# Kernel tuning notes

Hardware: AMD Instinct MI355X
Metric: run time of the kernel (lower is better)

Reference implementation:

```python
import jax, jax.numpy as jnp
import numpy as np

LANE_WEIGHT = 1.0   # _LANE_LOSS_WEIGHT
TEMP = 0.1          # args.score_temp

B, L, K, T = 256, 16, 64, 50
NL, NT = B * L, B * L * K


def _seg_ids(starts, n):
    # contiguous segments covering [0, n): segment id = (# starts <= i) - 1
    return (jnp.cumsum(jnp.zeros((n,), jnp.int32).at[starts].add(1)) - 1).astype(jnp.int32)


def _seg_log_softmax(x, seg, nseg):
    m = jax.ops.segment_max(x, seg, num_segments=nseg)
    z = x - m[seg]
    lse = jnp.log(jax.ops.segment_sum(jnp.exp(z), seg, num_segments=nseg))
    return z - lse[seg]


def _seg_softmax(x, seg, nseg):
    m = jax.ops.segment_max(x, seg, num_segments=nseg)
    e = jnp.exp(x - m[seg])
    s = jax.ops.segment_sum(e, seg, num_segments=nseg)
    return e / s[seg]


def setup_inputs() -> dict:
    key = jax.random.key(0)
    k1, k2, k3, k4, k5 = jax.random.split(key, 5)
    lane_scores = jax.random.normal(k1, (NL,), jnp.float32)
    traj_scores = jax.random.normal(k2, (NT, 1), jnp.float32)
    pred_candidates = jax.random.normal(k3, (NT, T, 2), jnp.float32)
    pred_gt = jax.random.normal(k4, (B, T, 2), jnp.float32)
    scales = jnp.ones((B,), jnp.float32)
    # ragged segment boundaries (here uniform, but reference only uses starts)
    cls_start_end_idx = jnp.stack([jnp.arange(B, dtype=jnp.int32) * L,
                                   jnp.arange(B, dtype=jnp.int32) * L + L], axis=1)
    trajs_start_end_idx = jnp.stack([jnp.arange(NL, dtype=jnp.int32) * K,
                                     jnp.arange(NL, dtype=jnp.int32) * K + K], axis=1)
    cls_oracle = jax.random.bernoulli(k5, 0.3, (NL,))
    # guarantee >= 1 oracle lane per sample (original divides by len(traj_loss))
    cls_oracle = cls_oracle.at[jnp.arange(B) * L].set(True)
    return {
        "lane_scores": lane_scores,
        "traj_scores": traj_scores,
        "pred_candidates": pred_candidates,
        "pred_gt": pred_gt,
        "scales": scales,
        "cls_oracle": cls_oracle,
        "cls_start_end_idx": cls_start_end_idx,
        "trajs_start_end_idx": trajs_start_end_idx,
    }


def reference(lane_scores, traj_scores, pred_candidates, pred_gt, scales,
              cls_oracle, cls_start_end_idx, trajs_start_end_idx):
    nl, nt = lane_scores.shape[0], traj_scores.shape[0]
    b = cls_start_end_idx.shape[0]
    lane_sample = _seg_ids(cls_start_end_idx[:, 0], nl)   # [NL] -> sample id
    traj_lane = _seg_ids(trajs_start_end_idx[:, 0], nt)   # [NT] -> lane id
    traj_sample = lane_sample[traj_lane]                  # [NT] -> sample id

    # ---- lane-level cross entropy per sample ----
    oracle_f = cls_oracle.astype(lane_scores.dtype)
    oracle_per_sample = jax.ops.segment_sum(oracle_f, lane_sample, num_segments=b)
    lane_target = oracle_f / oracle_per_sample[lane_sample]
    lane_logp = _seg_log_softmax(lane_scores, lane_sample, b)
    lane_loss = jax.ops.segment_sum(-lane_target * lane_logp, lane_sample,
                                    num_segments=b) * LANE_WEIGHT  # [B]

    # ---- trajectory-level cross entropy per oracle lane ----
    # ScoreEvaluator.scoring_trajs: ADE distance to GT, scale-normalized, negated
    diff = pred_candidates - pred_gt[traj_sample]          # [NT, T, 2]
    ade = jnp.mean(jnp.sqrt(jnp.sum(diff * diff, axis=-1) + 1e-12), axis=-1)
    scores = -ade / scales[traj_sample]                    # [NT]

    target = _seg_softmax(scores / TEMP, traj_lane, nl)    # softmax(scores/temp)
    out_logp = _seg_log_softmax(traj_scores[:, 0], traj_lane, nl)
    ce_per_lane = jax.ops.segment_sum(-target * out_logp, traj_lane,
                                      num_segments=nl)     # [NL]
    # only oracle lanes contribute; average over oracle-lane count per sample
    traj_loss = jax.ops.segment_sum(ce_per_lane * oracle_f, lane_sample,
                                    num_segments=b) / oracle_per_sample  # [B]

    return jnp.mean(lane_loss + traj_loss)
```

## Files before the change

### kernel.cpp

```cpp
#include <hip/hip_runtime.h>
#include <math.h>


#define LANE_WEIGHT 1.0f
#define TEMP_INV    10.0f

__global__ __launch_bounds__(256) void lane_ce_kernel(
    const float* __restrict__ pred_candidates,
    const float* __restrict__ pred_gt,
    const float* __restrict__ traj_scores,
    const float* __restrict__ scales,
    const int*   __restrict__ cls_se,
    const int*   __restrict__ trajs_se,
    float*       __restrict__ ws_ce,
    int B, int T)
{
    const int lane = blockIdx.x;
    const int tid  = threadIdx.x;

    __shared__ int    s_sample;
    __shared__ float4 s_gt4[64];
    __shared__ float  s_acc[64];

    if (tid == 0) {
        int lo = 0, hi = B - 1;
        while (lo < hi) {
            int mid = (lo + hi + 1) >> 1;
            if (cls_se[2 * mid] <= lane) lo = mid; else hi = mid - 1;
        }
        s_sample = lo;
    }
    __syncthreads();
    const int sample = s_sample;
    const int t0 = trajs_se[2 * lane];
    const int t1 = trajs_se[2 * lane + 1];
    const int Kl = t1 - t0;

    float* s_gt = (float*)s_gt4;
    for (int i = tid; i < T * 2; i += blockDim.x)
        s_gt[i] = pred_gt[(size_t)sample * (T * 2) + i];
    __syncthreads();

    const int tl = tid >> 2;
    const int q  = tid & 3;
    float partial = 0.0f;
    if (tl < Kl) {
        const float4* base =
            (const float4*)(pred_candidates + (size_t)(t0 + tl) * (T * 2));
        const int nf4 = T / 2;
        for (int r = q; r < nf4; r += 4) {
            float4 c = base[r];
            float4 g = s_gt4[r];
            float dx0 = c.x - g.x, dy0 = c.y - g.y;
            float dx1 = c.z - g.z, dy1 = c.w - g.w;
            partial += sqrtf(dx0 * dx0 + dy0 * dy0 + 1e-12f)
                     + sqrtf(dx1 * dx1 + dy1 * dy1 + 1e-12f);
        }
    }
    partial += __shfl_xor(partial, 1);
    partial += __shfl_xor(partial, 2);
    if (q == 0 && tl < Kl) s_acc[tl] = partial;
    __syncthreads();

    if (tid < 64) {
        const int  j     = tid;
        const bool valid = (j < Kl);
        const float inv_scale = 1.0f / scales[sample];

        float sc = valid ? (-(s_acc[j] / (float)T) * inv_scale * TEMP_INV)
                         : -INFINITY;
        float m = sc;
        for (int off = 32; off; off >>= 1) m = fmaxf(m, __shfl_xor(m, off));
        float e = valid ? expf(sc - m) : 0.0f;
        float Z = e;
        for (int off = 32; off; off >>= 1) Z += __shfl_xor(Z, off);
        float target = e / Z;

        float tsc = valid ? traj_scores[t0 + j] : -INFINITY;
        float m2 = tsc;
        for (int off = 32; off; off >>= 1) m2 = fmaxf(m2, __shfl_xor(m2, off));
        float e2 = valid ? expf(tsc - m2) : 0.0f;
        float Z2 = e2;
        for (int off = 32; off; off >>= 1) Z2 += __shfl_xor(Z2, off);
        float logp = (tsc - m2) - logf(Z2);

        float ce = valid ? (-target * logp) : 0.0f;
        for (int off = 32; off; off >>= 1) ce += __shfl_xor(ce, off);
        if (j == 0) ws_ce[lane] = ce;
    }
}

__global__ __launch_bounds__(256) void sample_loss_kernel(
    const float* __restrict__ lane_scores,
    const int*   __restrict__ cls_oracle,
    const int*   __restrict__ cls_se,
    const float* __restrict__ ws_ce,
    float*       __restrict__ out,
    int B)
{
    const int tid = threadIdx.x;
    float total = 0.0f;
    for (int s = tid; s < B; s += blockDim.x) {
        const int cs = cls_se[2 * s], ce_ = cls_se[2 * s + 1];
        float m = -INFINITY;
        for (int l = cs; l < ce_; ++l) m = fmaxf(m, lane_scores[l]);
        float Z = 0.0f; int cnt = 0;
        for (int l = cs; l < ce_; ++l) {
            Z += expf(lane_scores[l] - m);
            cnt += (cls_oracle[l] != 0);
        }
        const float lse = m + logf(Z);
        const float inv_cnt = 1.0f / (float)cnt;
        float lane_loss = 0.0f, traj_loss = 0.0f;
        for (int l = cs; l < ce_; ++l) {
            if (cls_oracle[l] != 0) {
                lane_loss += -(lane_scores[l] - lse);
                traj_loss += ws_ce[l];
            }
        }
        total += lane_loss * inv_cnt * LANE_WEIGHT + traj_loss * inv_cnt;
    }
    __shared__ float s_red[256];
    s_red[tid] = total;
    __syncthreads();
    for (int off = 128; off; off >>= 1) {
        if (tid < off) s_red[tid] += s_red[tid + off];
        __syncthreads();
    }
    if (tid == 0) out[0] = s_red[0] / (float)B;
}

extern "C" void kernel_launch(void* const* d_in, const int* in_sizes, int n_in,
                              void* d_out, int out_size, void* d_ws, size_t ws_size,
                              hipStream_t stream)
{
    const float* lane_scores     = (const float*)d_in[0];
    const float* traj_scores     = (const float*)d_in[1];
    const float* pred_candidates = (const float*)d_in[2];
    const float* pred_gt         = (const float*)d_in[3];
    const float* scales          = (const float*)d_in[4];
    const int*   cls_oracle      = (const int*)d_in[5];
    const int*   cls_se          = (const int*)d_in[6];
    const int*   trajs_se        = (const int*)d_in[7];

    const int NL = in_sizes[0];
    const int NT = in_sizes[1];
    const int B  = in_sizes[6] / 2;
    const int T  = in_sizes[2] / (NT * 2);

    float* ws_ce = (float*)d_ws;
    float* out   = (float*)d_out;

    lane_ce_kernel<<<NL, 256, 0, stream>>>(
        pred_candidates, pred_gt, traj_scores, scales,
        cls_se, trajs_se, ws_ce, B, T);

    sample_loss_kernel<<<1, 256, 0, stream>>>(
        lane_scores, cls_oracle, cls_se, ws_ce, out, B);
}
```

Measured before the change: 188.1 us.

## Map one wavefront per lane with one thread per trajectory

```diff
diff --git a/kernel.cpp b/kernel.cpp
--- a/kernel.cpp
+++ b/kernel.cpp
@@ -5,7 +5,7 @@
 #define LANE_WEIGHT 1.0f
 #define TEMP_INV    10.0f
 
-__global__ __launch_bounds__(256) void lane_ce_kernel(
+__global__ __launch_bounds__(256) void traj_ce_kernel(
     const float* __restrict__ pred_candidates,
     const float* __restrict__ pred_gt,
     const float* __restrict__ traj_scores,
@@ -13,81 +13,70 @@
     const int*   __restrict__ cls_se,
     const int*   __restrict__ trajs_se,
     float*       __restrict__ ws_ce,
-    int B, int T)
+    int B, int T, int NL)
 {
-    const int lane = blockIdx.x;
-    const int tid  = threadIdx.x;
+    const int wid     = threadIdx.x >> 6;
+    const int lane_id = threadIdx.x & 63;
+    const int lane    = blockIdx.x * 4 + wid;
+    if (lane >= NL) return;
 
-    __shared__ int    s_sample;
-    __shared__ float4 s_gt4[64];
-    __shared__ float  s_acc[64];
+    const int t0 = trajs_se[2 * lane];
+    const int Kl = trajs_se[2 * lane + 1] - t0;
 
-    if (tid == 0) {
-        int lo = 0, hi = B - 1;
-        while (lo < hi) {
-            int mid = (lo + hi + 1) >> 1;
-            if (cls_se[2 * mid] <= lane) lo = mid; else hi = mid - 1;
-        }
-        s_sample = lo;
+    int lo = 0, hi = B - 1;
+    while (lo < hi) {
+        int mid = (lo + hi + 1) >> 1;
+        if (cls_se[2 * mid] <= lane) lo = mid; else hi = mid - 1;
     }
-    __syncthreads();
-    const int sample = s_sample;
-    const int t0 = trajs_se[2 * lane];
-    const int t1 = trajs_se[2 * lane + 1];
-    const int Kl = t1 - t0;
+    const int sample = lo;
 
-    float* s_gt = (float*)s_gt4;
-    for (int i = tid; i < T * 2; i += blockDim.x)
-        s_gt[i] = pred_gt[(size_t)sample * (T * 2) + i];
-    __syncthreads();
+    const bool valid = (lane_id < Kl);
+    const int  traj  = t0 + (valid ? lane_id : (Kl > 0 ? Kl - 1 : 0));
 
-    const int tl = tid >> 2;
-    const int q  = tid & 3;
-    float partial = 0.0f;
-    if (tl < Kl) {
-        const float4* base =
-            (const float4*)(pred_candidates + (size_t)(t0 + tl) * (T * 2));
-        const int nf4 = T / 2;
-        for (int r = q; r < nf4; r += 4) {
-            float4 c = base[r];
-            float4 g = s_gt4[r];
-            float dx0 = c.x - g.x, dy0 = c.y - g.y;
-            float dx1 = c.z - g.z, dy1 = c.w - g.w;
-            partial += sqrtf(dx0 * dx0 + dy0 * dy0 + 1e-12f)
-                     + sqrtf(dx1 * dx1 + dy1 * dy1 + 1e-12f);
-        }
+    const float4* __restrict__ tp =
+        (const float4*)(pred_candidates + (size_t)traj * (T * 2));
+    const float4* __restrict__ gp =
+        (const float4*)(pred_gt + (size_t)sample * (T * 2));
+
+    const int nf4 = (T * 2) / 4;
+    float sum = 0.0f;
+    #pragma unroll 5
+    for (int r = 0; r < nf4; ++r) {
+        float4 c = tp[r];
+        float4 g = gp[r];
+        float dx0 = c.x - g.x, dy0 = c.y - g.y;
+        float dx1 = c.z - g.z, dy1 = c.w - g.w;
+        sum += sqrtf(dx0 * dx0 + dy0 * dy0 + 1e-12f)
+             + sqrtf(dx1 * dx1 + dy1 * dy1 + 1e-12f);
     }
-    partial += __shfl_xor(partial, 1);
-    partial += __shfl_xor(partial, 2);
-    if (q == 0 && tl < Kl) s_acc[tl] = partial;
-    __syncthreads();
+    if ((T & 1) != 0) {
+        const float2* tp2 = (const float2*)tp;
+        const float2* gp2 = (const float2*)gp;
+        float2 c = tp2[2 * nf4], g = gp2[2 * nf4];
+        float dx = c.x - g.x, dy = c.y - g.y;
+        sum += sqrtf(dx * dx + dy * dy + 1e-12f);
+    }
 
-    if (tid < 64) {
-        const int  j     = tid;
-        const bool valid = (j < Kl);
-        const float inv_scale = 1.0f / scales[sample];
+    const float inv_scale = 1.0f / scales[sample];
+    float sc = valid ? (-(sum / (float)T) * inv_scale * TEMP_INV) : -INFINITY;
+    float m = sc;
+    for (int off = 32; off; off >>= 1) m = fmaxf(m, __shfl_xor(m, off));
+    float e = valid ? expf(sc - m) : 0.0f;
+    float Z = e;
+    for (int off = 32; off; off >>= 1) Z += __shfl_xor(Z, off);
+    float target = e / Z;
 
-        float sc = valid ? (-(s_acc[j] / (float)T) * inv_scale * TEMP_INV)
-                         : -INFINITY;
-        float m = sc;
-        for (int off = 32; off; off >>= 1) m = fmaxf(m, __shfl_xor(m, off));
-        float e = valid ? expf(sc - m) : 0.0f;
-        float Z = e;
-        for (int off = 32; off; off >>= 1) Z += __shfl_xor(Z, off);
-        float target = e / Z;
+    float tsc = valid ? traj_scores[traj] : -INFINITY;
+    float m2 = tsc;
+    for (int off = 32; off; off >>= 1) m2 = fmaxf(m2, __shfl_xor(m2, off));
+    float e2 = valid ? expf(tsc - m2) : 0.0f;
+    float Z2 = e2;
+    for (int off = 32; off; off >>= 1) Z2 += __shfl_xor(Z2, off);
+    float logp = (tsc - m2) - logf(Z2);
 
-        float tsc = valid ? traj_scores[t0 + j] : -INFINITY;
-        float m2 = tsc;
-        for (int off = 32; off; off >>= 1) m2 = fmaxf(m2, __shfl_xor(m2, off));
-        float e2 = valid ? expf(tsc - m2) : 0.0f;
-        float Z2 = e2;
-        for (int off = 32; off; off >>= 1) Z2 += __shfl_xor(Z2, off);
-        float logp = (tsc - m2) - logf(Z2);
-
-        float ce = valid ? (-target * logp) : 0.0f;
-        for (int off = 32; off; off >>= 1) ce += __shfl_xor(ce, off);
-        if (j == 0) ws_ce[lane] = ce;
-    }
+    float ce = valid ? (-target * logp) : 0.0f;
+    for (int off = 32; off; off >>= 1) ce += __shfl_xor(ce, off);
+    if (lane_id == 0) ws_ce[lane] = ce;
 }
 
 __global__ __launch_bounds__(256) void sample_loss_kernel(
@@ -101,18 +90,18 @@
     const int tid = threadIdx.x;
     float total = 0.0f;
     for (int s = tid; s < B; s += blockDim.x) {
-        const int cs = cls_se[2 * s], ce_ = cls_se[2 * s + 1];
+        const int cs = cls_se[2 * s], cend = cls_se[2 * s + 1];
         float m = -INFINITY;
-        for (int l = cs; l < ce_; ++l) m = fmaxf(m, lane_scores[l]);
+        for (int l = cs; l < cend; ++l) m = fmaxf(m, lane_scores[l]);
         float Z = 0.0f; int cnt = 0;
-        for (int l = cs; l < ce_; ++l) {
+        for (int l = cs; l < cend; ++l) {
             Z += expf(lane_scores[l] - m);
             cnt += (cls_oracle[l] != 0);
         }
         const float lse = m + logf(Z);
         const float inv_cnt = 1.0f / (float)cnt;
         float lane_loss = 0.0f, traj_loss = 0.0f;
-        for (int l = cs; l < ce_; ++l) {
+        for (int l = cs; l < cend; ++l) {
             if (cls_oracle[l] != 0) {
                 lane_loss += -(lane_scores[l] - lse);
                 traj_loss += ws_ce[l];
@@ -151,9 +140,10 @@
     float* ws_ce = (float*)d_ws;
     float* out   = (float*)d_out;
 
-    lane_ce_kernel<<<NL, 256, 0, stream>>>(
+    const int nblocks = (NL + 3) / 4;
+    traj_ce_kernel<<<nblocks, 256, 0, stream>>>(
         pred_candidates, pred_gt, traj_scores, scales,
-        cls_se, trajs_se, ws_ce, B, T);
+        cls_se, trajs_se, ws_ce, B, T, NL);
 
     sample_loss_kernel<<<1, 256, 0, stream>>>(
         lane_scores, cls_oracle, cls_se, ws_ce, out, B);
```

After: 186.7 us. No clear change (-0.7%).
